# Kernel optimization log

Hardware: AMD Instinct MI355X
Metric: run time of the kernel (lower is better)

## Reference

```python
import jax, jax.numpy as jnp
import numpy as np

B, T, D, DFF, H, W = 2, 2048, 1024, 4096, 16, 512
HD = D // H
EPS = 1e-6
NEG = jnp.float32(-1e30)


def _rms(x, w):
    return x * jax.lax.rsqrt(jnp.mean(x * x, axis=-1, keepdims=True) + EPS) * w


def setup_inputs() -> dict:
    key = jax.random.key(0)
    ks = jax.random.split(key, 12)
    g = lambda k, shape, std: jax.random.normal(k, shape, jnp.float32) * std
    return {
        "x": jax.random.normal(ks[0], (B, T, D), jnp.float32),
        "retrieval_context": jax.random.normal(ks[1], (B, D), jnp.float32),
        "norm1_w": jnp.ones((D,), jnp.float32),
        "qkv_w": g(ks[2], (3 * D, D), 0.02),
        "qkv_b": jnp.zeros((3 * D,), jnp.float32),
        "proj_w": g(ks[3], (D, D), 0.02),
        "proj_b": jnp.zeros((D,), jnp.float32),
        "gate_w": g(ks[4], (3, D), 0.01),
        "gate_b": jnp.zeros((3,), jnp.float32),
        "ret_w": g(ks[5], (D, D), 0.01),
        "norm2_w": jnp.ones((D,), jnp.float32),
        "ffn_gate_w": g(ks[6], (DFF, D), 0.02),
        "ffn_up_w": g(ks[7], (DFF, D), 0.02),
        "ffn_down_w": g(ks[8], (D, DFF), 0.02),
    }


def reference(x, retrieval_context, norm1_w, qkv_w, qkv_b, proj_w, proj_b,
              gate_w, gate_b, ret_w, norm2_w, ffn_gate_w, ffn_up_w, ffn_down_w):
    # pre-norm
    h = _rms(x, norm1_w)  # (B,T,D)
    # qkv projection, split into heads
    qkv = h @ qkv_w.T + qkv_b  # (B,T,3D)
    q, k, v = jnp.split(qkv, 3, axis=-1)
    to_heads = lambda t: t.reshape(B, T, H, HD).transpose(0, 2, 1, 3)  # (B,H,T,HD)
    q, k, v = to_heads(q), to_heads(k), to_heads(v)
    # sliding-window causal mask: attend to j in [i-W+1, i]
    idx = jnp.arange(T)
    win = (idx[:, None] >= idx[None, :]) & (idx[:, None] - idx[None, :] < W)  # (T,T)
    scores = jnp.einsum("bhqd,bhkd->bhqk", q, k) / np.sqrt(HD).astype(np.float32)
    scores = jnp.where(win, scores, NEG)
    attn = jax.nn.softmax(scores, axis=-1)
    attn_out = jnp.einsum("bhqk,bhkd->bhqd", attn, v)  # (B,H,T,HD)
    attn_out = attn_out.transpose(0, 2, 1, 3).reshape(B, T, D)
    attn_out = attn_out @ proj_w.T + proj_b
    # retrieval stream (TRN disabled -> zeros, gate channel 1 hard-masked)
    ret_out = (retrieval_context @ ret_w.T)[:, None, :]  # (B,1,D) broadcast over T
    gate_logits = h @ gate_w.T + gate_b  # (B,T,3)
    gate_logits = gate_logits.at[:, :, 1].set(-1e9)  # enable_trn=False
    gates = jax.nn.softmax(gate_logits, axis=-1)
    mixed = gates[:, :, 0:1] * attn_out + gates[:, :, 2:3] * ret_out
    x = x + mixed
    # SwiGLU FFN
    h2 = _rms(x, norm2_w)
    ffn = (jax.nn.silu(h2 @ ffn_gate_w.T) * (h2 @ ffn_up_w.T)) @ ffn_down_w.T
    return x + ffn
```

## Files before the change

### kernel.cpp

```cpp
#include <hip/hip_runtime.h>
#include <hip/hip_bf16.h>

typedef __bf16 bf16_t;
typedef __bf16 bf16x8 __attribute__((ext_vector_type(8)));
typedef __bf16 bf16x4v __attribute__((ext_vector_type(4)));
typedef float f32x4 __attribute__((ext_vector_type(4)));

static constexpr int Bn = 2, Tn = 2048, Dn = 1024, DFFn = 4096, Hn = 16, HDn = 64, Wn = 512;
static constexpr int Mn = Bn * Tn;

#define MFMA16(a, b, c) __builtin_amdgcn_mfma_f32_16x16x32_bf16(a, b, c, 0, 0, 0)

typedef __attribute__((address_space(3))) void lds_void;
typedef const __attribute__((address_space(1))) void gbl_void;

__global__ __launch_bounds__(256) void cvt_f32_bf16_kernel(const float4* __restrict__ src,
                                                           bf16x4v* __restrict__ dst, int n4) {
  int i = blockIdx.x * 256 + threadIdx.x;
  if (i < n4) {
    float4 v = src[i];
    bf16x4v o;
    o[0] = (bf16_t)v.x; o[1] = (bf16_t)v.y; o[2] = (bf16_t)v.z; o[3] = (bf16_t)v.w;
    dst[i] = o;
  }
}

__device__ __forceinline__ float blockReduceSum(float v, float* sbuf) {
#pragma unroll
  for (int off = 32; off > 0; off >>= 1) v += __shfl_down(v, off, 64);
  int lane = threadIdx.x & 63, wid = threadIdx.x >> 6;
  __syncthreads();
  if (lane == 0) sbuf[wid] = v;
  __syncthreads();
  return sbuf[0] + sbuf[1] + sbuf[2] + sbuf[3];
}

template <bool GATE>
__global__ __launch_bounds__(256) void rmsnorm_kernel(const float* __restrict__ x,
                                                      const float* __restrict__ w,
                                                      bf16_t* __restrict__ out,
                                                      const float* __restrict__ gw,
                                                      const float* __restrict__ gb,
                                                      float* __restrict__ gates) {
  __shared__ float sbuf[4];
  int row = blockIdx.x, tid = threadIdx.x;
  const float4* xr = (const float4*)(x + (long)row * Dn);
  float4 v = xr[tid];
  float ss = v.x * v.x + v.y * v.y + v.z * v.z + v.w * v.w;
  ss = blockReduceSum(ss, sbuf);
  float rms = rsqrtf(ss * (1.0f / Dn) + 1e-6f);
  float4 wv = ((const float4*)w)[tid];
  float h0 = v.x * rms * wv.x, h1 = v.y * rms * wv.y;
  float h2 = v.z * rms * wv.z, h3 = v.w * rms * wv.w;
  bf16x4v o;
  o[0] = (bf16_t)h0; o[1] = (bf16_t)h1; o[2] = (bf16_t)h2; o[3] = (bf16_t)h3;
  ((bf16x4v*)(out + (long)row * Dn))[tid] = o;
  if (GATE) {
    float4 g0v = ((const float4*)gw)[tid];
    float4 g2v = ((const float4*)(gw + 2 * Dn))[tid];
    float l0 = h0 * g0v.x + h1 * g0v.y + h2 * g0v.z + h3 * g0v.w;
    float l2 = h0 * g2v.x + h1 * g2v.y + h2 * g2v.z + h3 * g2v.w;
    l0 = blockReduceSum(l0, sbuf);
    l2 = blockReduceSum(l2, sbuf);
    if (tid == 0) {
      l0 += gb[0];
      l2 += gb[2];
      float mx = fmaxf(l0, l2);
      float e0 = __expf(l0 - mx), e2 = __expf(l2 - mx);
      float inv = 1.0f / (e0 + e2);
      gates[2 * row] = e0 * inv;
      gates[2 * row + 1] = e2 * inv;
    }
  }
}

template <int EPI>
__global__ __launch_bounds__(256) void gemm_kernel(const bf16_t* __restrict__ A,
                                                   const bf16_t* __restrict__ Wt, int K, int N,
                                                   const float* __restrict__ bias,
                                                   bf16_t* __restrict__ outb,
                                                   float* __restrict__ outf,
                                                   const float* __restrict__ gates,
                                                   const float* __restrict__ ret,
                                                   const float* __restrict__ resid) {
  __shared__ bf16_t smem[8192];
  const int tid = threadIdx.x;
  const int w = tid >> 6, lane = tid & 63;
  const int wr = w >> 1, wc = w & 1;
  const int m0 = blockIdx.y * 128, n0 = blockIdx.x * 128;

  const bf16_t* gsrc[4];
#pragma unroll
  for (int q = 0; q < 4; q++) {
    int e = ((w * 4 + q) * 64 + lane) * 8;
    int rr = (e & 4095) >> 5, cc = e & 31;
    gsrc[q] = (e < 4096) ? (A + (long)(m0 + rr) * K + cc) : (Wt + (long)(n0 + rr) * K + cc);
  }
  bf16_t* lbase = &smem[(w * 4) * 512];

  f32x4 acc[4][4];
#pragma unroll
  for (int i = 0; i < 4; i++)
#pragma unroll
    for (int j = 0; j < 4; j++) acc[i][j] = (f32x4){0.f, 0.f, 0.f, 0.f};

  const int lr = lane & 15, lc = (lane >> 4) * 8;

  for (int kt = 0; kt < K; kt += 32) {
    if (kt) __syncthreads();
#pragma unroll
    for (int q = 0; q < 4; q++) {
      __builtin_amdgcn_global_load_lds((gbl_void*)(gsrc[q] + kt), (lds_void*)(lbase + q * 512), 16,
                                       0, 0);
    }
    __syncthreads();

    bf16x8 af[4], bfv[4];
#pragma unroll
    for (int i = 0; i < 4; i++) af[i] = *(const bf16x8*)&smem[(wr * 64 + i * 16 + lr) * 32 + lc];
#pragma unroll
    for (int i = 0; i < 4; i++)
      bfv[i] = *(const bf16x8*)&smem[4096 + (wc * 64 + i * 16 + lr) * 32 + lc];
#pragma unroll
    for (int mi = 0; mi < 4; mi++)
#pragma unroll
      for (int ni = 0; ni < 4; ni++) acc[mi][ni] = MFMA16(af[mi], bfv[ni], acc[mi][ni]);
  }

  const int lrow4 = (lane >> 4) * 4;
#pragma unroll
  for (int mi = 0; mi < 4; mi++) {
#pragma unroll
    for (int rr2 = 0; rr2 < 4; rr2++) {
      int r = m0 + wr * 64 + mi * 16 + lrow4 + rr2;
      float g0 = 0.f, g2 = 0.f;
      const float* retb = nullptr;
      if (EPI == 2) {
        g0 = gates[2 * r];
        g2 = gates[2 * r + 1];
        retb = ret + ((r >> 11) << 10);
      }
#pragma unroll
      for (int ni = 0; ni < 4; ni++) {
        int c = n0 + wc * 64 + ni * 16 + (lane & 15);
        float v = acc[mi][ni][rr2];
        long idx = (long)r * N + c;
        if (EPI == 0) {
          if (bias) v += bias[c];
          outb[idx] = (bf16_t)v;
        } else if (EPI == 2) {
          outf[idx] = resid[idx] + g0 * (v + bias[c]) + g2 * retb[c];
        } else {
          outf[idx] = resid[idx] + v;
        }
      }
    }
  }
}

__global__ __launch_bounds__(256) void retproj_kernel(const float* __restrict__ rc,
                                                      const float* __restrict__ rw,
                                                      float* __restrict__ out) {
  int gw = blockIdx.x * 4 + (threadIdx.x >> 6);
  int lane = threadIdx.x & 63;
  int b = gw >> 10, n = gw & 1023;
  float v = 0.f;
  for (int k = lane; k < Dn; k += 64) v += rc[b * Dn + k] * rw[(long)n * Dn + k];
#pragma unroll
  for (int off = 32; off > 0; off >>= 1) v += __shfl_down(v, off, 64);
  if (lane == 0) out[gw] = v;
}

__global__ __launch_bounds__(256) void attn_kernel(const bf16_t* __restrict__ qkv,
                                                   bf16_t* __restrict__ out) {
  __shared__ bf16_t psh[4][512];
  const int tid = threadIdx.x, w = tid >> 6, lane = tid & 63;
  const int qb = blockIdx.x, bh = blockIdx.y;
  const int b = bh >> 4, h = bh & 15;
  const int qw0 = qb * 64 + w * 16;
  const bf16_t* base = qkv + (long)b * Tn * 3072 + h * 64;
  const bf16_t* kb = base + Dn;
  const bf16_t* vb = base + 2 * Dn;
  const int lr = lane & 15, lg = lane >> 4;

  bf16x8 aq0 = *(const bf16x8*)(base + (long)(qw0 + lr) * 3072 + lg * 8);
  bf16x8 aq1 = *(const bf16x8*)(base + (long)(qw0 + lr) * 3072 + lg * 8 + 32);

  float m_run[4], l_run[4];
  f32x4 accv[4];
#pragma unroll
  for (int r = 0; r < 4; r++) { m_run[r] = -1e30f; l_run[r] = 0.f; }
#pragma unroll
  for (int c = 0; c < 4; c++) accv[c] = (f32x4){0.f, 0.f, 0.f, 0.f};

  int j_lo = qw0 - (Wn - 1);
  if (j_lo < 0) j_lo = 0;
  j_lo &= ~31;
  const int j_hi = qw0 + 15;

  for (int j0 = j_lo; j0 <= j_hi; j0 += 32) {
    f32x4 s[2];
#pragma unroll
    for (int hh = 0; hh < 2; hh++) {
      const bf16_t* kr = kb + (long)(j0 + hh * 16 + lr) * 3072 + lg * 8;
      bf16x8 k0 = *(const bf16x8*)kr;
      bf16x8 k1 = *(const bf16x8*)(kr + 32);
      f32x4 z = (f32x4){0.f, 0.f, 0.f, 0.f};
      z = MFMA16(aq0, k0, z);
      z = MFMA16(aq1, k1, z);
      s[hh] = z;
    }
    float mt[4];
#pragma unroll
    for (int r = 0; r < 4; r++) {
      int q = qw0 + lg * 4 + r;
      int c0 = j0 + lr, c1 = j0 + 16 + lr;
      float s0 = (q >= c0 && (q - c0) < Wn) ? s[0][r] * 0.125f : -1e30f;
      float s1 = (q >= c1 && (q - c1) < Wn) ? s[1][r] * 0.125f : -1e30f;
      s[0][r] = s0;
      s[1][r] = s1;
      mt[r] = fmaxf(s0, s1);
    }
#pragma unroll
    for (int off = 1; off < 16; off <<= 1)
#pragma unroll
      for (int r = 0; r < 4; r++) mt[r] = fmaxf(mt[r], __shfl_xor(mt[r], off, 64));
    float rs[4];
#pragma unroll
    for (int r = 0; r < 4; r++) {
      float nm = fmaxf(m_run[r], mt[r]);
      float alpha = __expf(m_run[r] - nm);
      m_run[r] = nm;
      float p0 = __expf(s[0][r] - nm);
      float p1 = __expf(s[1][r] - nm);
      psh[w][(lg * 4 + r) * 32 + lr] = (bf16_t)p0;
      psh[w][(lg * 4 + r) * 32 + 16 + lr] = (bf16_t)p1;
      rs[r] = p0 + p1;
      l_run[r] *= alpha;
#pragma unroll
      for (int c = 0; c < 4; c++) accv[c][r] *= alpha;
    }
#pragma unroll
    for (int off = 1; off < 16; off <<= 1)
#pragma unroll
      for (int r = 0; r < 4; r++) rs[r] += __shfl_xor(rs[r], off, 64);
#pragma unroll
    for (int r = 0; r < 4; r++) l_run[r] += rs[r];

    bf16x8 ap = *(const bf16x8*)&psh[w][lr * 32 + lg * 8];
#pragma unroll
    for (int c = 0; c < 4; c++) {
      bf16x8 bv;
#pragma unroll
      for (int jj = 0; jj < 8; jj++) bv[jj] = vb[(long)(j0 + lg * 8 + jj) * 3072 + c * 16 + lr];
      accv[c] = MFMA16(ap, bv, accv[c]);
    }
  }
#pragma unroll
  for (int r = 0; r < 4; r++) {
    float inv = 1.0f / l_run[r];
    long orow = ((long)b * Tn + qw0 + lg * 4 + r) * Dn + h * 64;
#pragma unroll
    for (int c = 0; c < 4; c++) out[orow + c * 16 + lr] = (bf16_t)(accv[c][r] * inv);
  }
}

__global__ __launch_bounds__(256) void silu_mul_kernel(const bf16_t* __restrict__ gu,
                                                       bf16_t* __restrict__ act) {
  int m = blockIdx.y;
  int j0 = (blockIdx.x * 256 + threadIdx.x) * 8;
  bf16x8 g = *(const bf16x8*)(gu + (long)m * (2 * DFFn) + j0);
  bf16x8 u = *(const bf16x8*)(gu + (long)m * (2 * DFFn) + DFFn + j0);
  bf16x8 o;
#pragma unroll
  for (int i = 0; i < 8; i++) {
    float gf = (float)g[i], uf = (float)u[i];
    float sf = gf / (1.0f + __expf(-gf));
    o[i] = (bf16_t)(sf * uf);
  }
  *(bf16x8*)(act + (long)m * DFFn + j0) = o;
}

extern "C" void kernel_launch(void* const* d_in, const int* in_sizes, int n_in, void* d_out,
                              int out_size, void* d_ws, size_t ws_size, hipStream_t stream) {
  const float* x = (const float*)d_in[0];
  const float* rc = (const float*)d_in[1];
  const float* n1w = (const float*)d_in[2];
  const float* qkv_w = (const float*)d_in[3];
  const float* qkv_b = (const float*)d_in[4];
  const float* proj_w = (const float*)d_in[5];
  const float* proj_b = (const float*)d_in[6];
  const float* gate_w = (const float*)d_in[7];
  const float* gate_b = (const float*)d_in[8];
  const float* ret_w = (const float*)d_in[9];
  const float* n2w = (const float*)d_in[10];
  const float* fgw = (const float*)d_in[11];
  const float* fuw = (const float*)d_in[12];
  const float* fdw = (const float*)d_in[13];
  float* out = (float*)d_out;

  char* ws = (char*)d_ws;
  size_t off = 0;
  auto alloc = [&](size_t bytes) {
    char* p = ws + off;
    off += (bytes + 255) & ~(size_t)255;
    return p;
  };
  bf16_t* wqkv = (bf16_t*)alloc(3072l * 1024 * 2);
  bf16_t* wproj = (bf16_t*)alloc(1024l * 1024 * 2);
  bf16_t* wgup = (bf16_t*)alloc(8192l * 1024 * 2);
  bf16_t* wdown = (bf16_t*)alloc(1024l * 4096 * 2);
  bf16_t* h1 = (bf16_t*)alloc((long)Mn * 1024 * 2);
  bf16_t* h2 = (bf16_t*)alloc((long)Mn * 1024 * 2);
  bf16_t* qkvb = (bf16_t*)alloc((long)Mn * 3072 * 2);
  bf16_t* attnb = (bf16_t*)alloc((long)Mn * 1024 * 2);
  bf16_t* gupo = (bf16_t*)alloc((long)Mn * 8192 * 2);
  bf16_t* actb = (bf16_t*)alloc((long)Mn * 4096 * 2);
  float* gates = (float*)alloc((long)Mn * 2 * 4);
  float* retb = (float*)alloc(2048 * 4);
  float* xmid = (float*)alloc((long)Mn * 1024 * 4);

  cvt_f32_bf16_kernel<<<3072, 256, 0, stream>>>((const float4*)qkv_w, (bf16x4v*)wqkv, 786432);
  cvt_f32_bf16_kernel<<<1024, 256, 0, stream>>>((const float4*)proj_w, (bf16x4v*)wproj, 262144);
  cvt_f32_bf16_kernel<<<4096, 256, 0, stream>>>((const float4*)fgw, (bf16x4v*)wgup, 1048576);
  cvt_f32_bf16_kernel<<<4096, 256, 0, stream>>>((const float4*)fuw, (bf16x4v*)(wgup + 4194304),
                                                1048576);
  cvt_f32_bf16_kernel<<<4096, 256, 0, stream>>>((const float4*)fdw, (bf16x4v*)wdown, 1048576);

  rmsnorm_kernel<true><<<Mn, 256, 0, stream>>>(x, n1w, h1, gate_w, gate_b, gates);
  gemm_kernel<0><<<dim3(24, 32), 256, 0, stream>>>(h1, wqkv, 1024, 3072, qkv_b, qkvb, nullptr,
                                                   nullptr, nullptr, nullptr);
  retproj_kernel<<<512, 256, 0, stream>>>(rc, ret_w, retb);
  attn_kernel<<<dim3(32, 32), 256, 0, stream>>>(qkvb, attnb);
  gemm_kernel<2><<<dim3(8, 32), 256, 0, stream>>>(attnb, wproj, 1024, 1024, proj_b, nullptr, xmid,
                                                  gates, retb, x);
  rmsnorm_kernel<false><<<Mn, 256, 0, stream>>>(xmid, n2w, h2, nullptr, nullptr, nullptr);
  gemm_kernel<0><<<dim3(64, 32), 256, 0, stream>>>(h2, wgup, 1024, 8192, nullptr, gupo, nullptr,
                                                   nullptr, nullptr, nullptr);
  silu_mul_kernel<<<dim3(2, 4096), 256, 0, stream>>>(gupo, actb);
  gemm_kernel<3><<<dim3(8, 32), 256, 0, stream>>>(actb, wdown, 4096, 1024, nullptr, nullptr, out,
                                                  nullptr, nullptr, xmid);
}
```

Baseline: 494.9 us.

## Add 256x256-tile pipelined GEMM for QKV and gate/up projections

Introduces a new GEMM kernel with 256x256 output tiles, 8 waves, double-buffered LDS filled via direct global-to-LDS loads, and phased MFMA interleaved with prefetch plus setprio. It replaces the 128x128 GEMM for the QKV projection and the fused gate/up projection. The goal is higher arithmetic intensity per block and better overlap of loads with matrix math. In exchange it uses 128KB of LDS and many accumulator registers, and the QKV launch has only 192 blocks, which may underfill the GPU.

After: 486.5 us. Within noise of the previous version (-1.7%).

```diff
diff --git a/kernel.cpp b/kernel.cpp
--- a/kernel.cpp
+++ b/kernel.cpp
@@ -74,6 +74,139 @@
   }
 }
 
+__global__ __launch_bounds__(512, 2) void gemm256_kernel(const bf16_t* __restrict__ Ag,
+                                                         const bf16_t* __restrict__ Wt, int K,
+                                                         int N, const float* __restrict__ bias,
+                                                         bf16_t* __restrict__ outb) {
+  __shared__ bf16_t lds2[65536];
+  const int tid = threadIdx.x;
+  const int wid = tid >> 6, lane = tid & 63;
+  const int wr = wid >> 2, wc = wid & 3;
+  const int m0 = blockIdx.y * 256, n0 = blockIdx.x * 256;
+  const int lr = lane & 15, lg = lane >> 4;
+  const int lterm = (lr * 32 + lg * 8) ^ (((lr >> 3) & 1) << 4);
+  const int colsw = (lane & 3) * 8 ^ (((lane >> 5) & 1) << 4);
+  const int NT = K >> 6;
+
+  auto stageA = [&](int buf, int half, int t) {
+#pragma unroll
+    for (int q = 0; q < 2; q++) {
+      int s = q * 8 + wid, s_r = s >> 1, s_c = s & 1;
+      const bf16_t* src =
+          Ag + (long)(m0 + half * 128 + s_r * 16 + (lane >> 2)) * K + (long)t * 64 + s_c * 32 + colsw;
+      bf16_t* dst = &lds2[buf * 32768 + (half * 8 + s_r) * 1024 + s_c * 512];
+      __builtin_amdgcn_global_load_lds((gbl_void*)src, (lds_void*)dst, 16, 0, 0);
+    }
+  };
+  auto stageB = [&](int buf, int half, int t) {
+#pragma unroll
+    for (int q = 0; q < 2; q++) {
+      int s = q * 8 + wid, s_r = s >> 1, s_c = s & 1;
+      const bf16_t* src =
+          Wt + (long)(n0 + half * 128 + s_r * 16 + (lane >> 2)) * K + (long)t * 64 + s_c * 32 + colsw;
+      bf16_t* dst = &lds2[buf * 32768 + 16384 + (half * 8 + s_r) * 1024 + s_c * 512];
+      __builtin_amdgcn_global_load_lds((gbl_void*)src, (lds_void*)dst, 16, 0, 0);
+    }
+  };
+
+  f32x4 acc[8][4];
+#pragma unroll
+  for (int i = 0; i < 8; i++)
+#pragma unroll
+    for (int j = 0; j < 4; j++) acc[i][j] = (f32x4){0.f, 0.f, 0.f, 0.f};
+
+  stageB(0, 0, 0);
+  stageB(0, 1, 0);
+  stageA(0, 0, 0);
+  stageA(0, 1, 0);
+  if (NT > 1) {
+    stageB(1, 0, 1);
+    stageB(1, 1, 1);
+    asm volatile("s_waitcnt vmcnt(4)" ::: "memory");
+  } else {
+    asm volatile("s_waitcnt vmcnt(0)" ::: "memory");
+  }
+  __builtin_amdgcn_sched_barrier(0);
+  __builtin_amdgcn_s_barrier();
+
+#define LDA(mi, ks) (*(const bf16x8*)&lds2[ca + ((wr << 3) + (mi)) * 1024 + (ks)*512 + lterm])
+#define LDB(ni, ks) (*(const bf16x8*)&lds2[cb + ((wc << 2) + (ni)) * 1024 + (ks)*512 + lterm])
+
+#define GPHASE(mi0, ...)                                                                  \
+  do {                                                                                    \
+    bf16x8 a0k0 = LDA(mi0, 0), a0k1 = LDA(mi0, 1);                                        \
+    bf16x8 a1k0 = LDA((mi0) + 1, 0), a1k1 = LDA((mi0) + 1, 1);                            \
+    __VA_ARGS__;                                                                          \
+    __builtin_amdgcn_s_barrier();                                                         \
+    asm volatile("s_waitcnt lgkmcnt(0)" ::: "memory");                                    \
+    __builtin_amdgcn_sched_barrier(0);                                                    \
+    __builtin_amdgcn_s_setprio(1);                                                        \
+    _Pragma("unroll") for (int ni = 0; ni < 4; ni++) {                                    \
+      acc[mi0][ni] = MFMA16(a0k0, bfr[ni][0], acc[mi0][ni]);                              \
+      acc[mi0][ni] = MFMA16(a0k1, bfr[ni][1], acc[mi0][ni]);                              \
+      acc[(mi0) + 1][ni] = MFMA16(a1k0, bfr[ni][0], acc[(mi0) + 1][ni]);                  \
+      acc[(mi0) + 1][ni] = MFMA16(a1k1, bfr[ni][1], acc[(mi0) + 1][ni]);                  \
+    }                                                                                     \
+    __builtin_amdgcn_s_setprio(0);                                                        \
+    __builtin_amdgcn_s_barrier();                                                         \
+  } while (0)
+
+#define GTILE(t, cur)                                                                     \
+  do {                                                                                    \
+    const int ca = (cur)*32768, cb = ca + 16384;                                          \
+    bf16x8 bfr[4][2];                                                                     \
+    _Pragma("unroll") for (int ni = 0; ni < 4; ni++) {                                    \
+      bfr[ni][0] = LDB(ni, 0);                                                            \
+      bfr[ni][1] = LDB(ni, 1);                                                            \
+    }                                                                                     \
+    GPHASE(0, {                                                                           \
+      if ((t) + 1 < NT) {                                                                 \
+        stageA(1 - (cur), 0, (t) + 1);                                                    \
+        stageA(1 - (cur), 1, (t) + 1);                                                    \
+      }                                                                                   \
+    });                                                                                   \
+    GPHASE(2, {                                                                           \
+      if ((t) + 2 < NT) stageB((cur), 0, (t) + 2);                                        \
+    });                                                                                   \
+    GPHASE(4, {                                                                           \
+      if ((t) + 2 < NT) stageB((cur), 1, (t) + 2);                                        \
+    });                                                                                   \
+    GPHASE(6, {});                                                                        \
+    if ((t) + 1 < NT) {                                                                   \
+      if ((t) + 2 < NT)                                                                   \
+        asm volatile("s_waitcnt vmcnt(4)" ::: "memory");                                  \
+      else                                                                                \
+        asm volatile("s_waitcnt vmcnt(0)" ::: "memory");                                  \
+      __builtin_amdgcn_sched_barrier(0);                                                  \
+      __builtin_amdgcn_s_barrier();                                                       \
+    }                                                                                     \
+  } while (0)
+
+  for (int t = 0; t < NT; t += 2) {
+    GTILE(t, 0);
+    GTILE(t + 1, 1);
+  }
+
+#pragma unroll
+  for (int mi = 0; mi < 8; mi++) {
+#pragma unroll
+    for (int rr = 0; rr < 4; rr++) {
+      long r = m0 + wr * 128 + mi * 16 + lg * 4 + rr;
+#pragma unroll
+      for (int ni = 0; ni < 4; ni++) {
+        int c = n0 + wc * 64 + ni * 16 + lr;
+        float v = acc[mi][ni][rr];
+        if (bias) v += bias[c];
+        outb[r * N + c] = (bf16_t)v;
+      }
+    }
+  }
+#undef LDA
+#undef LDB
+#undef GPHASE
+#undef GTILE
+}
+
 template <int EPI>
 __global__ __launch_bounds__(256) void gemm_kernel(const bf16_t* __restrict__ A,
                                                    const bf16_t* __restrict__ Wt, int K, int N,
@@ -328,15 +461,13 @@
   cvt_f32_bf16_kernel<<<4096, 256, 0, stream>>>((const float4*)fdw, (bf16x4v*)wdown, 1048576);
 
   rmsnorm_kernel<true><<<Mn, 256, 0, stream>>>(x, n1w, h1, gate_w, gate_b, gates);
-  gemm_kernel<0><<<dim3(24, 32), 256, 0, stream>>>(h1, wqkv, 1024, 3072, qkv_b, qkvb, nullptr,
-                                                   nullptr, nullptr, nullptr);
+  gemm256_kernel<<<dim3(12, 16), 512, 0, stream>>>(h1, wqkv, 1024, 3072, qkv_b, qkvb);
   retproj_kernel<<<512, 256, 0, stream>>>(rc, ret_w, retb);
   attn_kernel<<<dim3(32, 32), 256, 0, stream>>>(qkvb, attnb);
   gemm_kernel<2><<<dim3(8, 32), 256, 0, stream>>>(attnb, wproj, 1024, 1024, proj_b, nullptr, xmid,
                                                   gates, retb, x);
   rmsnorm_kernel<false><<<Mn, 256, 0, stream>>>(xmid, n2w, h2, nullptr, nullptr, nullptr);
-  gemm_kernel<0><<<dim3(64, 32), 256, 0, stream>>>(h2, wgup, 1024, 8192, nullptr, gupo, nullptr,
-                                                   nullptr, nullptr, nullptr);
+  gemm256_kernel<<<dim3(32, 16), 512, 0, stream>>>(h2, wgup, 1024, 8192, nullptr, gupo);
   silu_mul_kernel<<<dim3(2, 4096), 256, 0, stream>>>(gupo, actb);
   gemm_kernel<3><<<dim3(8, 32), 256, 0, stream>>>(actb, wdown, 4096, 1024, nullptr, nullptr, out,
                                                   nullptr, nullptr, xmid);
```
